# Kernel tuning notes

Hardware: AMD Instinct MI355X
Metric: run time of the kernel (lower is better)

## Reference

```python
import jax, jax.numpy as jnp
import numpy as np

N_NODES = 50000
N_EDGES = 1250000
IN_CH, HID_CH, OUT_CH = 128, 64, 10
N_GRAPHS = 500


def gcn_conv(x, W, src, dst, n_nodes):
    # GCNConv (bias=False, normalize=True, add_self_loops=True):
    # out = D^{-1/2} (A + I) D^{-1/2} X W
    h = x @ W  # [N, H]
    loop = jnp.arange(n_nodes, dtype=src.dtype)
    s = jnp.concatenate([src, loop])
    d = jnp.concatenate([dst, loop])
    deg = jax.ops.segment_sum(jnp.ones_like(d, dtype=h.dtype), d, num_segments=n_nodes)
    dinv = jnp.where(deg > 0, jax.lax.rsqrt(deg), 0.0)
    norm = dinv[s] * dinv[d]  # [E+N]
    msgs = h[s] * norm[:, None]  # gather + normalize
    return jax.ops.segment_sum(msgs, d, num_segments=n_nodes)  # scatter-add


def setup_inputs() -> dict:
    key = jax.random.key(0)
    ks = jax.random.split(key, 8)
    x = jax.random.normal(ks[0], (N_NODES, IN_CH), dtype=jnp.float32)
    edge_index = jax.random.randint(ks[1], (2, N_EDGES), 0, N_NODES, dtype=jnp.int64)
    batch = jnp.sort(jax.random.randint(ks[2], (N_NODES,), 0, N_GRAPHS, dtype=jnp.int64))
    def glorot(k, fan_in, fan_out):
        lim = np.sqrt(6.0 / (fan_in + fan_out))
        return jax.random.uniform(k, (fan_in, fan_out), jnp.float32, -lim, lim)
    W1 = glorot(ks[3], IN_CH, HID_CH)
    W2 = glorot(ks[4], HID_CH, HID_CH)
    W3 = glorot(ks[5], HID_CH, HID_CH)
    Wl = glorot(ks[6], HID_CH, OUT_CH)
    bl = jnp.zeros((OUT_CH,), jnp.float32)
    return {"x": x, "edge_index": edge_index, "batch": batch,
            "W1": W1, "W2": W2, "W3": W3, "Wl": Wl, "bl": bl}


def reference(x, edge_index, batch, W1, W2, W3, Wl, bl):
    src, dst = edge_index[0], edge_index[1]
    n = x.shape[0]
    h = jax.nn.relu(gcn_conv(x, W1, src, dst, n))
    h = jax.nn.relu(gcn_conv(h, W2, src, dst, n))
    h = gcn_conv(h, W3, src, dst, n)
    # global_mean_pool over graph ids
    sums = jax.ops.segment_sum(h, batch, num_segments=N_GRAPHS)
    cnts = jax.ops.segment_sum(jnp.ones((n,), h.dtype), batch, num_segments=N_GRAPHS)
    pooled = sums / jnp.maximum(cnts, 1.0)[:, None]
    return pooled @ Wl + bl
```

## Files before the change

### kernel.cpp

```cpp
#include <hip/hip_runtime.h>

#define CH 64
#define CHUNK 4096
#define BSHIFT 8
#define NBUCK 196

__device__ __forceinline__ unsigned short f2bf_rne(float f) {
    unsigned int u = __float_as_uint(f);
    u += 0x7fffu + ((u >> 16) & 1u);
    return (unsigned short)(u >> 16);
}
__device__ __forceinline__ float bf_lo(unsigned int q) {
    return __uint_as_float(q << 16);
}
__device__ __forceinline__ float bf_hi(unsigned int q) {
    return __uint_as_float(q & 0xffff0000u);
}

__global__ __launch_bounds__(256) void bucket_hist_kernel(
        const int* __restrict__ dst, int* __restrict__ bucket_cnt, int E) {
    __shared__ int hist[256];
    int tid = threadIdx.x;
    int e0 = blockIdx.x * CHUNK;
    int total = min(CHUNK, E - e0);
    hist[tid] = 0;
    __syncthreads();
    for (int i = tid; i < total; i += 256)
        atomicAdd(&hist[dst[e0 + i] >> BSHIFT], 1);
    __syncthreads();
    if (tid < NBUCK && hist[tid]) atomicAdd(&bucket_cnt[tid], hist[tid]);
}

__global__ __launch_bounds__(256) void bucket_scan_kernel(
        const int* __restrict__ cnt, int* __restrict__ base,
        int* __restrict__ cursor, int* __restrict__ rowptr, int N, int E) {
    __shared__ int sc[256];
    int tid = threadIdx.x;
    int c = (tid < NBUCK) ? cnt[tid] : 0;
    sc[tid] = c;
    __syncthreads();
    for (int off = 1; off < 256; off <<= 1) {
        int v = (tid >= off) ? sc[tid - off] : 0;
        __syncthreads();
        sc[tid] += v;
        __syncthreads();
    }
    if (tid < NBUCK) { base[tid] = sc[tid] - c; cursor[tid] = sc[tid] - c; }
    if (tid == NBUCK - 1) base[NBUCK] = sc[tid];
    if (tid == 0) rowptr[N] = E;
}

__global__ __launch_bounds__(256) void bin_kernel(
        const int* __restrict__ src, const int* __restrict__ dst,
        int* __restrict__ cursor, int2* __restrict__ pairs, int E) {
    __shared__ int2 stage[CHUNK];
    __shared__ int hist[256], sc[256], lbase[256], lcur[256], gbase[256];
    int tid = threadIdx.x;
    int e0 = blockIdx.x * CHUNK;
    int total = min(CHUNK, E - e0);
    hist[tid] = 0;
    __syncthreads();
    for (int i = tid; i < total; i += 256)
        atomicAdd(&hist[dst[e0 + i] >> BSHIFT], 1);
    __syncthreads();
    sc[tid] = hist[tid];
    __syncthreads();
    for (int off = 1; off < 256; off <<= 1) {
        int v = (tid >= off) ? sc[tid - off] : 0;
        __syncthreads();
        sc[tid] += v;
        __syncthreads();
    }
    lbase[tid] = sc[tid] - hist[tid];
    lcur[tid]  = sc[tid] - hist[tid];
    if (tid < NBUCK && hist[tid] > 0) gbase[tid] = atomicAdd(&cursor[tid], hist[tid]);
    __syncthreads();
    for (int i = tid; i < total; i += 256) {
        int s = src[e0 + i], d = dst[e0 + i];
        int pos = atomicAdd(&lcur[d >> BSHIFT], 1);
        stage[pos] = make_int2(s, d);
    }
    __syncthreads();
    for (int i = tid; i < total; i += 256) {
        int2 p = stage[i];
        int b = p.y >> BSHIFT;
        pairs[gbase[b] + (i - lbase[b])] = p;
    }
}

__global__ __launch_bounds__(256) void bucket_sort_kernel(
        const int2* __restrict__ pairs, const int* __restrict__ base,
        int* __restrict__ csr, int* __restrict__ rowptr,
        float* __restrict__ dinv, int N) {
    __shared__ int cntl[256], sc[256], cur[256];
    int tid = threadIdx.x;
    int b = blockIdx.x;
    int lo = b << BSHIFT;
    int pbase = base[b], pend = base[b + 1];
    int cnt = pend - pbase;
    cntl[tid] = 0;
    __syncthreads();
    for (int i = tid; i < cnt; i += 256)
        atomicAdd(&cntl[pairs[pbase + i].y - lo], 1);
    __syncthreads();
    sc[tid] = cntl[tid];
    __syncthreads();
    for (int off = 1; off < 256; off <<= 1) {
        int v = (tid >= off) ? sc[tid - off] : 0;
        __syncthreads();
        sc[tid] += v;
        __syncthreads();
    }
    int excl = sc[tid] - cntl[tid];
    cur[tid] = excl;
    int v = lo + tid;
    if (v < N) {
        rowptr[v] = pbase + excl;
        dinv[v] = rsqrtf((float)(cntl[tid] + 1));
    }
    __syncthreads();
    for (int i = tid; i < cnt; i += 256) {
        int2 p = pairs[pbase + i];
        int pos = atomicAdd(&cur[p.y - lo], 1);
        csr[pbase + pos] = p.x;
    }
}

template <int K>
__global__ __launch_bounds__(256) void gemm_scale_kernel(
        const float* __restrict__ X, const float* __restrict__ W,
        const float* __restrict__ dinv, unsigned short* __restrict__ G, int N) {
    constexpr int KC  = 64;
    constexpr int XLD = KC + 4;
    __shared__ float Xs[64 * XLD];
    __shared__ float Wls[KC * CH];
    int tid = threadIdx.x;
    int tx  = tid & 15;
    int ty  = tid >> 4;
    int row_tile = blockIdx.x * 64;
    int r0 = ty * 4;
    float acc[4][4] = {{0.f}};

    for (int kc = 0; kc < K; kc += KC) {
        __syncthreads();
#pragma unroll
        for (int t = 0; t < 4; ++t) {
            int idx = tid + t * 256;
            int row = idx >> 4;
            int k4  = idx & 15;
            int grow = row_tile + row;
            const float4* xs = (const float4*)(X + (size_t)min(grow, N - 1) * K + kc);
            *(float4*)&Xs[row * XLD + 4 * k4] = xs[k4];
        }
#pragma unroll
        for (int t = 0; t < 4; ++t) {
            int idx = tid + t * 256;
            *(float4*)&Wls[idx * 4] = ((const float4*)(W + (size_t)kc * CH))[idx];
        }
        __syncthreads();
#pragma unroll
        for (int kk = 0; kk < KC; kk += 4) {
            float xr[4][4], wr[4][4];
#pragma unroll
            for (int i = 0; i < 4; ++i) {
                float4 v = *(const float4*)&Xs[(r0 + i) * XLD + kk];
                xr[i][0] = v.x; xr[i][1] = v.y; xr[i][2] = v.z; xr[i][3] = v.w;
            }
#pragma unroll
            for (int j = 0; j < 4; ++j) {
                float4 v = *(const float4*)&Wls[(kk + j) * CH + 4 * tx];
                wr[j][0] = v.x; wr[j][1] = v.y; wr[j][2] = v.z; wr[j][3] = v.w;
            }
#pragma unroll
            for (int i = 0; i < 4; ++i)
#pragma unroll
                for (int j = 0; j < 4; ++j)
#pragma unroll
                    for (int c = 0; c < 4; ++c)
                        acc[i][c] = fmaf(xr[i][j], wr[j][c], acc[i][c]);
        }
    }
#pragma unroll
    for (int i = 0; i < 4; ++i) {
        int r = row_tile + r0 + i;
        if (r < N) {
            float d = dinv[r];
            ushort4 o;
            o.x = f2bf_rne(acc[i][0] * d);
            o.y = f2bf_rne(acc[i][1] * d);
            o.z = f2bf_rne(acc[i][2] * d);
            o.w = f2bf_rne(acc[i][3] * d);
            ((ushort4*)G)[(size_t)r * 16 + tx] = o;
        }
    }
}

__global__ __launch_bounds__(256) void aggregate_kernel(
        const unsigned short* __restrict__ G, const int* __restrict__ rowptr,
        const int* __restrict__ csr, const float* __restrict__ dinv,
        float* __restrict__ Out, int N, int relu) {
    int lane = threadIdx.x & 63;
    int v = (blockIdx.x * 256 + threadIdx.x) >> 6;
    if (v >= N) return;
    int grp = lane >> 3;
    int cl  = lane & 7;
    const uint4* __restrict__ G4 = (const uint4*)G;

    int beg = rowptr[v], end = rowptr[v + 1];
    float a0 = 0.f, a1 = 0.f, a2 = 0.f, a3 = 0.f;
    float a4 = 0.f, a5 = 0.f, a6 = 0.f, a7 = 0.f;
#pragma unroll 2
    for (int e = beg; e < end; e += 8) {
        int eg = e + grp;
        int raw = csr[eg];
        bool ok = eg < end;
        int u = ok ? raw : 0;
        float s = ok ? 1.f : 0.f;
        uint4 q = G4[(size_t)u * 8 + cl];
        a0 = fmaf(bf_lo(q.x), s, a0); a1 = fmaf(bf_hi(q.x), s, a1);
        a2 = fmaf(bf_lo(q.y), s, a2); a3 = fmaf(bf_hi(q.y), s, a3);
        a4 = fmaf(bf_lo(q.z), s, a4); a5 = fmaf(bf_hi(q.z), s, a5);
        a6 = fmaf(bf_lo(q.w), s, a6); a7 = fmaf(bf_hi(q.w), s, a7);
    }
#pragma unroll
    for (int off = 8; off <= 32; off <<= 1) {
        a0 += __shfl_xor(a0, off); a1 += __shfl_xor(a1, off);
        a2 += __shfl_xor(a2, off); a3 += __shfl_xor(a3, off);
        a4 += __shfl_xor(a4, off); a5 += __shfl_xor(a5, off);
        a6 += __shfl_xor(a6, off); a7 += __shfl_xor(a7, off);
    }

    if (lane < 8) {
        uint4 q = G4[(size_t)v * 8 + lane];
        float d = dinv[v];
        float o0 = (a0 + bf_lo(q.x)) * d, o1 = (a1 + bf_hi(q.x)) * d;
        float o2 = (a2 + bf_lo(q.y)) * d, o3 = (a3 + bf_hi(q.y)) * d;
        float o4 = (a4 + bf_lo(q.z)) * d, o5 = (a5 + bf_hi(q.z)) * d;
        float o6 = (a6 + bf_lo(q.w)) * d, o7 = (a7 + bf_hi(q.w)) * d;
        if (relu) {
            o0 = fmaxf(o0, 0.f); o1 = fmaxf(o1, 0.f); o2 = fmaxf(o2, 0.f);
            o3 = fmaxf(o3, 0.f); o4 = fmaxf(o4, 0.f); o5 = fmaxf(o5, 0.f);
            o6 = fmaxf(o6, 0.f); o7 = fmaxf(o7, 0.f);
        }
        float4 w0 = {o0, o1, o2, o3}, w1 = {o4, o5, o6, o7};
        ((float4*)Out)[(size_t)v * 16 + lane * 2]     = w0;
        ((float4*)Out)[(size_t)v * 16 + lane * 2 + 1] = w1;
    }
}

__global__ void gptr_kernel(const int* __restrict__ batch, int* __restrict__ gptr,
                            int N, int NG) {
    int g = blockIdx.x * blockDim.x + threadIdx.x;
    if (g > NG) return;
    if (g == NG) { gptr[NG] = N; return; }
    int lo = 0, hi = N;
    while (lo < hi) {
        int mid = (lo + hi) >> 1;
        if (batch[mid] < g) lo = mid + 1; else hi = mid;
    }
    gptr[g] = lo;
}

__global__ __launch_bounds__(64) void pool_head_kernel(
        const float* __restrict__ H, const int* __restrict__ gptr,
        const float* __restrict__ Wl, const float* __restrict__ bl,
        float* __restrict__ out, int NG) {
    int g = blockIdx.x;
    int lane = threadIdx.x;
    int s = gptr[g], e = gptr[g + 1];
    float acc = 0.f;
    for (int v = s; v < e; ++v) acc += H[(size_t)v * CH + lane];
    float c = (float)(e - s);
    float mean = (c > 0.f) ? acc / c : 0.f;
    for (int o = 0; o < 10; ++o) {
        float t = mean * Wl[lane * 10 + o];
        for (int off = 32; off > 0; off >>= 1) t += __shfl_down(t, off);
        if (lane == 0) out[g * 10 + o] = t + bl[o];
    }
}

extern "C" void kernel_launch(void* const* d_in, const int* in_sizes, int n_in,
                              void* d_out, int out_size, void* d_ws, size_t ws_size,
                              hipStream_t stream) {
    const float* x     = (const float*)d_in[0];
    const int*   ei    = (const int*)d_in[1];
    const int*   batch = (const int*)d_in[2];
    const float* W1    = (const float*)d_in[3];
    const float* W2    = (const float*)d_in[4];
    const float* W3    = (const float*)d_in[5];
    const float* Wl    = (const float*)d_in[6];
    const float* bl    = (const float*)d_in[7];
    float* out = (float*)d_out;

    const int N  = in_sizes[0] / 128;
    const int E  = in_sizes[1] / 2;
    const int NG = out_size / 10;

    const int* src = ei;
    const int* dst = ei + E;

    char* ws = (char*)d_ws;
    size_t off = 0;
    auto alloc = [&](size_t bytes) -> void* {
        void* p = ws + off;
        off += bytes;
        off = (off + 255) & ~(size_t)255;
        return p;
    };
    int*   bucket_cnt    = (int*)alloc((size_t)NBUCK * 4);
    int*   bucket_base   = (int*)alloc((size_t)(NBUCK + 1) * 4);
    int*   bucket_cursor = (int*)alloc((size_t)NBUCK * 4);
    int*   csr    = (int*)alloc((size_t)(E + 16) * 4);
    int*   rowptr = (int*)alloc((size_t)(N + 1) * 4);
    float* dinv   = (float*)alloc((size_t)N * 4);
    int*   gptr   = (int*)alloc((size_t)(NG + 1) * 4);
    unsigned short* Gbf = (unsigned short*)alloc((size_t)N * CH * 2);
    float* hbuf   = (float*)alloc((size_t)N * CH * 4);
    int2*  pairs  = (int2*)hbuf;

    hipMemsetAsync(bucket_cnt, 0, (size_t)NBUCK * 4, stream);

    int cb = (E + CHUNK - 1) / CHUNK;
    int wb = (N + 3) / 4;
    int gb = (N + 63) / 64;

    bucket_hist_kernel<<<cb, 256, 0, stream>>>(dst, bucket_cnt, E);
    bucket_scan_kernel<<<1, 256, 0, stream>>>(bucket_cnt, bucket_base, bucket_cursor,
                                              rowptr, N, E);
    bin_kernel<<<cb, 256, 0, stream>>>(src, dst, bucket_cursor, pairs, E);
    bucket_sort_kernel<<<NBUCK, 256, 0, stream>>>(pairs, bucket_base, csr, rowptr, dinv, N);
    gptr_kernel<<<(NG + 512) / 512, 512, 0, stream>>>(batch, gptr, N, NG);

    gemm_scale_kernel<128><<<gb, 256, 0, stream>>>(x, W1, dinv, Gbf, N);
    aggregate_kernel<<<wb, 256, 0, stream>>>(Gbf, rowptr, csr, dinv, hbuf, N, 1);
    gemm_scale_kernel<64><<<gb, 256, 0, stream>>>(hbuf, W2, dinv, Gbf, N);
    aggregate_kernel<<<wb, 256, 0, stream>>>(Gbf, rowptr, csr, dinv, hbuf, N, 1);
    gemm_scale_kernel<64><<<gb, 256, 0, stream>>>(hbuf, W3, dinv, Gbf, N);
    aggregate_kernel<<<wb, 256, 0, stream>>>(Gbf, rowptr, csr, dinv, hbuf, N, 0);

    pool_head_kernel<<<NG, 64, 0, stream>>>(hbuf, gptr, Wl, bl, out, NG);
}
```

Before: 247.4 us.

## Pack edge pairs into 32 bits, store hidden features as bf16, remap aggregation lanes

```diff
diff --git a/kernel.cpp b/kernel.cpp
--- a/kernel.cpp
+++ b/kernel.cpp
@@ -16,6 +16,9 @@
 __device__ __forceinline__ float bf_hi(unsigned int q) {
     return __uint_as_float(q & 0xffff0000u);
 }
+__device__ __forceinline__ unsigned int pack2bf(float lo, float hi) {
+    return (unsigned int)f2bf_rne(lo) | ((unsigned int)f2bf_rne(hi) << 16);
+}
 
 __global__ __launch_bounds__(256) void bucket_hist_kernel(
         const int* __restrict__ dst, int* __restrict__ bucket_cnt, int E) {
@@ -52,8 +55,8 @@
 
 __global__ __launch_bounds__(256) void bin_kernel(
         const int* __restrict__ src, const int* __restrict__ dst,
-        int* __restrict__ cursor, int2* __restrict__ pairs, int E) {
-    __shared__ int2 stage[CHUNK];
+        int* __restrict__ cursor, unsigned int* __restrict__ pairs, int E) {
+    __shared__ unsigned int stage[CHUNK];
     __shared__ int hist[256], sc[256], lbase[256], lcur[256], gbase[256];
     int tid = threadIdx.x;
     int e0 = blockIdx.x * CHUNK;
@@ -76,32 +79,32 @@
     if (tid < NBUCK && hist[tid] > 0) gbase[tid] = atomicAdd(&cursor[tid], hist[tid]);
     __syncthreads();
     for (int i = tid; i < total; i += 256) {
-        int s = src[e0 + i], d = dst[e0 + i];
+        unsigned int s = (unsigned int)src[e0 + i];
+        unsigned int d = (unsigned int)dst[e0 + i];
         int pos = atomicAdd(&lcur[d >> BSHIFT], 1);
-        stage[pos] = make_int2(s, d);
+        stage[pos] = (d << 16) | s;
     }
     __syncthreads();
     for (int i = tid; i < total; i += 256) {
-        int2 p = stage[i];
-        int b = p.y >> BSHIFT;
+        unsigned int p = stage[i];
+        int b = (int)(p >> 24);
         pairs[gbase[b] + (i - lbase[b])] = p;
     }
 }
 
 __global__ __launch_bounds__(256) void bucket_sort_kernel(
-        const int2* __restrict__ pairs, const int* __restrict__ base,
+        const unsigned int* __restrict__ pairs, const int* __restrict__ base,
         int* __restrict__ csr, int* __restrict__ rowptr,
         float* __restrict__ dinv, int N) {
     __shared__ int cntl[256], sc[256], cur[256];
     int tid = threadIdx.x;
     int b = blockIdx.x;
-    int lo = b << BSHIFT;
     int pbase = base[b], pend = base[b + 1];
     int cnt = pend - pbase;
     cntl[tid] = 0;
     __syncthreads();
     for (int i = tid; i < cnt; i += 256)
-        atomicAdd(&cntl[pairs[pbase + i].y - lo], 1);
+        atomicAdd(&cntl[(pairs[pbase + i] >> 16) & 255u], 1);
     __syncthreads();
     sc[tid] = cntl[tid];
     __syncthreads();
@@ -113,21 +116,21 @@
     }
     int excl = sc[tid] - cntl[tid];
     cur[tid] = excl;
-    int v = lo + tid;
+    int v = (b << BSHIFT) + tid;
     if (v < N) {
         rowptr[v] = pbase + excl;
         dinv[v] = rsqrtf((float)(cntl[tid] + 1));
     }
     __syncthreads();
     for (int i = tid; i < cnt; i += 256) {
-        int2 p = pairs[pbase + i];
-        int pos = atomicAdd(&cur[p.y - lo], 1);
-        csr[pbase + pos] = p.x;
+        unsigned int p = pairs[pbase + i];
+        int pos = atomicAdd(&cur[(p >> 16) & 255u], 1);
+        csr[pbase + pos] = (int)(p & 0xffffu);
     }
 }
 
 template <int K>
-__global__ __launch_bounds__(256) void gemm_scale_kernel(
+__global__ __launch_bounds__(256) void gemm_f32_kernel(
         const float* __restrict__ X, const float* __restrict__ W,
         const float* __restrict__ dinv, unsigned short* __restrict__ G, int N) {
     constexpr int KC  = 64;
@@ -195,26 +198,98 @@
     }
 }
 
+__global__ __launch_bounds__(256) void gemm_bf16_kernel(
+        const unsigned short* __restrict__ Xbf, const float* __restrict__ W,
+        const float* __restrict__ dinv, unsigned short* __restrict__ G, int N) {
+    constexpr int XLDU = 36;
+    __shared__ unsigned int Xs[64 * XLDU];
+    __shared__ float Wls[64 * CH];
+    int tid = threadIdx.x;
+    int tx  = tid & 15;
+    int ty  = tid >> 4;
+    int row_tile = blockIdx.x * 64;
+    int r0 = ty * 4;
+    float acc[4][4] = {{0.f}};
+
+#pragma unroll
+    for (int t = 0; t < 2; ++t) {
+        int idx = tid + t * 256;
+        int row = idx >> 3;
+        int k4  = idx & 7;
+        int grow = row_tile + row;
+        uint4 v = ((const uint4*)Xbf)[(size_t)min(grow, N - 1) * 8 + k4];
+        *(uint4*)&Xs[row * XLDU + 4 * k4] = v;
+    }
+#pragma unroll
+    for (int t = 0; t < 4; ++t) {
+        int idx = tid + t * 256;
+        *(float4*)&Wls[idx * 4] = ((const float4*)W)[idx];
+    }
+    __syncthreads();
+#pragma unroll
+    for (int kk = 0; kk < 64; kk += 4) {
+        float xr[4][4], wr[4][4];
+#pragma unroll
+        for (int i = 0; i < 4; ++i) {
+            uint2 q = *(const uint2*)&Xs[(r0 + i) * XLDU + (kk >> 1)];
+            xr[i][0] = bf_lo(q.x); xr[i][1] = bf_hi(q.x);
+            xr[i][2] = bf_lo(q.y); xr[i][3] = bf_hi(q.y);
+        }
+#pragma unroll
+        for (int j = 0; j < 4; ++j) {
+            float4 v = *(const float4*)&Wls[(kk + j) * CH + 4 * tx];
+            wr[j][0] = v.x; wr[j][1] = v.y; wr[j][2] = v.z; wr[j][3] = v.w;
+        }
+#pragma unroll
+        for (int i = 0; i < 4; ++i)
+#pragma unroll
+            for (int j = 0; j < 4; ++j)
+#pragma unroll
+                for (int c = 0; c < 4; ++c)
+                    acc[i][c] = fmaf(xr[i][j], wr[j][c], acc[i][c]);
+    }
+#pragma unroll
+    for (int i = 0; i < 4; ++i) {
+        int r = row_tile + r0 + i;
+        if (r < N) {
+            float d = dinv[r];
+            ushort4 o;
+            o.x = f2bf_rne(acc[i][0] * d);
+            o.y = f2bf_rne(acc[i][1] * d);
+            o.z = f2bf_rne(acc[i][2] * d);
+            o.w = f2bf_rne(acc[i][3] * d);
+            ((ushort4*)G)[(size_t)r * 16 + tx] = o;
+        }
+    }
+}
+
+template <bool F32OUT>
 __global__ __launch_bounds__(256) void aggregate_kernel(
         const unsigned short* __restrict__ G, const int* __restrict__ rowptr,
         const int* __restrict__ csr, const float* __restrict__ dinv,
-        float* __restrict__ Out, int N, int relu) {
+        void* __restrict__ Out, int N, int E, int relu) {
     int lane = threadIdx.x & 63;
-    int v = (blockIdx.x * 256 + threadIdx.x) >> 6;
-    if (v >= N) return;
+    int w = (blockIdx.x * 256 + threadIdx.x) >> 6;
     int grp = lane >> 3;
     int cl  = lane & 7;
+    int v = w * 8 + grp;
+    bool valid = v < N;
+    int vc = valid ? v : N - 1;
+    int beg = rowptr[vc];
+    int cnt = valid ? rowptr[vc + 1] - beg : 0;
+    int mx = cnt;
+    mx = max(mx, __shfl_xor(mx, 8));
+    mx = max(mx, __shfl_xor(mx, 16));
+    mx = max(mx, __shfl_xor(mx, 32));
+
     const uint4* __restrict__ G4 = (const uint4*)G;
-
-    int beg = rowptr[v], end = rowptr[v + 1];
     float a0 = 0.f, a1 = 0.f, a2 = 0.f, a3 = 0.f;
     float a4 = 0.f, a5 = 0.f, a6 = 0.f, a7 = 0.f;
 #pragma unroll 2
-    for (int e = beg; e < end; e += 8) {
-        int eg = e + grp;
-        int raw = csr[eg];
-        bool ok = eg < end;
-        int u = ok ? raw : 0;
+    for (int it = 0; it < mx; ++it) {
+        int eg = min(beg + it, E - 1);
+        bool ok = it < cnt;
+        int u = ok ? csr[eg] : 0;
         float s = ok ? 1.f : 0.f;
         uint4 q = G4[(size_t)u * 8 + cl];
         a0 = fmaf(bf_lo(q.x), s, a0); a1 = fmaf(bf_hi(q.x), s, a1);
@@ -222,16 +297,8 @@
         a4 = fmaf(bf_lo(q.z), s, a4); a5 = fmaf(bf_hi(q.z), s, a5);
         a6 = fmaf(bf_lo(q.w), s, a6); a7 = fmaf(bf_hi(q.w), s, a7);
     }
-#pragma unroll
-    for (int off = 8; off <= 32; off <<= 1) {
-        a0 += __shfl_xor(a0, off); a1 += __shfl_xor(a1, off);
-        a2 += __shfl_xor(a2, off); a3 += __shfl_xor(a3, off);
-        a4 += __shfl_xor(a4, off); a5 += __shfl_xor(a5, off);
-        a6 += __shfl_xor(a6, off); a7 += __shfl_xor(a7, off);
-    }
-
-    if (lane < 8) {
-        uint4 q = G4[(size_t)v * 8 + lane];
+    if (valid) {
+        uint4 q = G4[(size_t)v * 8 + cl];
         float d = dinv[v];
         float o0 = (a0 + bf_lo(q.x)) * d, o1 = (a1 + bf_hi(q.x)) * d;
         float o2 = (a2 + bf_lo(q.y)) * d, o3 = (a3 + bf_hi(q.y)) * d;
@@ -242,9 +309,16 @@
             o3 = fmaxf(o3, 0.f); o4 = fmaxf(o4, 0.f); o5 = fmaxf(o5, 0.f);
             o6 = fmaxf(o6, 0.f); o7 = fmaxf(o7, 0.f);
         }
-        float4 w0 = {o0, o1, o2, o3}, w1 = {o4, o5, o6, o7};
-        ((float4*)Out)[(size_t)v * 16 + lane * 2]     = w0;
-        ((float4*)Out)[(size_t)v * 16 + lane * 2 + 1] = w1;
+        if (F32OUT) {
+            float4 w0 = {o0, o1, o2, o3}, w1 = {o4, o5, o6, o7};
+            ((float4*)Out)[(size_t)v * 16 + cl * 2]     = w0;
+            ((float4*)Out)[(size_t)v * 16 + cl * 2 + 1] = w1;
+        } else {
+            uint4 p;
+            p.x = pack2bf(o0, o1); p.y = pack2bf(o2, o3);
+            p.z = pack2bf(o4, o5); p.w = pack2bf(o6, o7);
+            ((uint4*)Out)[(size_t)v * 8 + cl] = p;
+        }
     }
 }
 
@@ -310,18 +384,19 @@
     int*   bucket_cnt    = (int*)alloc((size_t)NBUCK * 4);
     int*   bucket_base   = (int*)alloc((size_t)(NBUCK + 1) * 4);
     int*   bucket_cursor = (int*)alloc((size_t)NBUCK * 4);
-    int*   csr    = (int*)alloc((size_t)(E + 16) * 4);
+    int*   csr    = (int*)alloc((size_t)(E + 64) * 4);
     int*   rowptr = (int*)alloc((size_t)(N + 1) * 4);
     float* dinv   = (float*)alloc((size_t)N * 4);
     int*   gptr   = (int*)alloc((size_t)(NG + 1) * 4);
     unsigned short* Gbf = (unsigned short*)alloc((size_t)N * CH * 2);
+    unsigned short* Hbf = (unsigned short*)alloc((size_t)N * CH * 2);
     float* hbuf   = (float*)alloc((size_t)N * CH * 4);
-    int2*  pairs  = (int2*)hbuf;
+    unsigned int* pairs = (unsigned int*)hbuf;
 
     hipMemsetAsync(bucket_cnt, 0, (size_t)NBUCK * 4, stream);
 
     int cb = (E + CHUNK - 1) / CHUNK;
-    int wb = (N + 3) / 4;
+    int ab = ((N + 7) / 8 + 3) / 4;
     int gb = (N + 63) / 64;
 
     bucket_hist_kernel<<<cb, 256, 0, stream>>>(dst, bucket_cnt, E);
@@ -331,12 +406,12 @@
     bucket_sort_kernel<<<NBUCK, 256, 0, stream>>>(pairs, bucket_base, csr, rowptr, dinv, N);
     gptr_kernel<<<(NG + 512) / 512, 512, 0, stream>>>(batch, gptr, N, NG);
 
-    gemm_scale_kernel<128><<<gb, 256, 0, stream>>>(x, W1, dinv, Gbf, N);
-    aggregate_kernel<<<wb, 256, 0, stream>>>(Gbf, rowptr, csr, dinv, hbuf, N, 1);
-    gemm_scale_kernel<64><<<gb, 256, 0, stream>>>(hbuf, W2, dinv, Gbf, N);
-    aggregate_kernel<<<wb, 256, 0, stream>>>(Gbf, rowptr, csr, dinv, hbuf, N, 1);
-    gemm_scale_kernel<64><<<gb, 256, 0, stream>>>(hbuf, W3, dinv, Gbf, N);
-    aggregate_kernel<<<wb, 256, 0, stream>>>(Gbf, rowptr, csr, dinv, hbuf, N, 0);
+    gemm_f32_kernel<128><<<gb, 256, 0, stream>>>(x, W1, dinv, Gbf, N);
+    aggregate_kernel<false><<<ab, 256, 0, stream>>>(Gbf, rowptr, csr, dinv, Hbf, N, E, 1);
+    gemm_bf16_kernel<<<gb, 256, 0, stream>>>(Hbf, W2, dinv, Gbf, N);
+    aggregate_kernel<false><<<ab, 256, 0, stream>>>(Gbf, rowptr, csr, dinv, Hbf, N, E, 1);
+    gemm_bf16_kernel<<<gb, 256, 0, stream>>>(Hbf, W3, dinv, Gbf, N);
+    aggregate_kernel<true><<<ab, 256, 0, stream>>>(Gbf, rowptr, csr, dinv, hbuf, N, E, 0);
 
     pool_head_kernel<<<NG, 64, 0, stream>>>(hbuf, gptr, Wl, bl, out, NG);
 }
```

Measured after the change: 251.2 us. No clear change (+1.6%).
